# Kernel tuning notes

Measured on AMD Instinct MI355X. Metric: run time of the kernel, lower is better.

## Reference

```python
import jax, jax.numpy as jnp
import numpy as np

B, S, D = 4, 2048, 1024
H = 16
HD = D // H  # 64
MASKED_BIAS = jnp.float32(-10000.0)


def setup_inputs() -> dict:
    key = jax.random.key(0)
    ks = jax.random.split(key, 5)
    std = 0.02
    return {
        "hidden_states": jax.random.normal(ks[0], (B, S, D), jnp.float32),
        "Wq": jax.random.normal(ks[1], (D, D), jnp.float32) * std,
        "bq": jnp.zeros((D,), jnp.float32),
        "Wk": jax.random.normal(ks[2], (D, D), jnp.float32) * std,
        "bk": jnp.zeros((D,), jnp.float32),
        "Wv": jax.random.normal(ks[3], (D, D), jnp.float32) * std,
        "bv": jnp.zeros((D,), jnp.float32),
        "Wo": jax.random.normal(ks[4], (D, D), jnp.float32) * std,
        "bo": jnp.zeros((D,), jnp.float32),
    }


def _split_heads(x):
    # [B, S, D] -> [B, H, S, HD]
    return x.reshape(B, S, H, HD).transpose(0, 2, 1, 3)


def reference(hidden_states, Wq, bq, Wk, bk, Wv, bv, Wo, bo):
    q = _split_heads(hidden_states @ Wq + bq)
    k = _split_heads(hidden_states @ Wk + bk)
    v = _split_heads(hidden_states @ Wv + bv)

    # scores [B, H, S, S], scaled by sqrt(head_dim) (scale=True)
    w = jnp.einsum("bhqd,bhkd->bhqk", q, k) / jnp.sqrt(jnp.float32(HD))
    causal = jnp.tril(jnp.ones((S, S), dtype=bool))  # [S, S]
    w = jnp.where(causal[None, None], w, MASKED_BIAS)
    w = jax.nn.softmax(w, axis=-1)
    # attn_pdrop = 0.0 -> dropout is identity

    a = jnp.einsum("bhqk,bhkd->bhqd", w, v)  # [B, H, S, HD]
    a = a.transpose(0, 2, 1, 3).reshape(B, S, D)  # merge heads
    out = a @ Wo + bo
    # resid_pdrop = 0.0 -> identity
    return out
```

## Files before the change

### kernel.cpp

```cpp
#include <hip/hip_runtime.h>
#include <stdint.h>

typedef unsigned short u16;
typedef __bf16 bf16x2 __attribute__((ext_vector_type(2)));
typedef __bf16 bf16x8 __attribute__((ext_vector_type(8)));
typedef float f32x4 __attribute__((ext_vector_type(4)));
typedef float f32x16 __attribute__((ext_vector_type(16)));
typedef unsigned int u32x4 __attribute__((ext_vector_type(4)));
typedef u16 u16x8 __attribute__((ext_vector_type(8)));
typedef u16 u16x4 __attribute__((ext_vector_type(4)));

#define MFMA16(a, b, c) __builtin_amdgcn_mfma_f32_16x16x32_bf16((a), (b), (c), 0, 0, 0)
#define MFMA32(a, b, c) __builtin_amdgcn_mfma_f32_32x32x16_bf16((a), (b), (c), 0, 0, 0)

#define QSCALE 0.18033688011112042f

#if defined(__has_builtin)
#if __has_builtin(__builtin_amdgcn_exp2f)
#define EXP2(x) __builtin_amdgcn_exp2f(x)
#endif
#endif
#ifndef EXP2
#define EXP2(x) __expf((x) * 0.6931471805599453f)
#endif

__device__ __forceinline__ u16 f2bf(float f) {
  return __builtin_bit_cast(u16, (__bf16)f);
}

__device__ __forceinline__ unsigned cvtpk(float lo, float hi) {
  bf16x2 t;
  t[0] = (__bf16)lo;
  t[1] = (__bf16)hi;
  return __builtin_bit_cast(unsigned, t);
}

__device__ __forceinline__ bf16x8 load_frag(const u16* lds_base, int byteoff) {
  u32x4 v = *(const u32x4*)((const char*)lds_base + byteoff);
  return __builtin_bit_cast(bf16x8, v);
}

#define GLOAD_LDS16(gp, lp)                                                        \
  __builtin_amdgcn_global_load_lds((const __attribute__((address_space(1))) void*)(gp), \
                                   (__attribute__((address_space(3))) void*)(lp), 16, 0, 0)

template <int ROWS>
__device__ __forceinline__ void stage_tile(const u16* __restrict__ src, int ld, u16* lds,
                                           int tid) {
  constexpr int SLOTS = ROWS * 8;
#pragma unroll
  for (int it = 0; it < SLOTS / 256; ++it) {
    const int s = it * 256 + tid;
    const int row = s >> 3;
    const int seg = (s & 7) ^ (row & 7);
    const u16* g = src + row * ld + seg * 8;
    u16* l = lds + (it * 256 + (tid & ~63)) * 8;
    GLOAD_LDS16(g, l);
  }
}


__global__ __launch_bounds__(256) void cvt_x(const float* __restrict__ in,
                                             u16* __restrict__ out) {
  const int i = (int)blockIdx.x * 256 + (int)threadIdx.x;
  const float4 a = ((const float4*)in)[2 * i];
  const float4 b = ((const float4*)in)[2 * i + 1];
  u16x8 o;
  o[0] = f2bf(a.x); o[1] = f2bf(a.y); o[2] = f2bf(a.z); o[3] = f2bf(a.w);
  o[4] = f2bf(b.x); o[5] = f2bf(b.y); o[6] = f2bf(b.z); o[7] = f2bf(b.w);
  ((u16x8*)out)[i] = o;
}

__global__ __launch_bounds__(256) void cvt_w_t4(const float* __restrict__ W0,
                                                const float* __restrict__ W1,
                                                const float* __restrict__ W2,
                                                const float* __restrict__ W3,
                                                u16* __restrict__ T0, u16* __restrict__ T1,
                                                u16* __restrict__ T2, u16* __restrict__ T3) {
  const int z = (int)blockIdx.z;
  const float* W = z == 0 ? W0 : (z == 1 ? W1 : (z == 2 ? W2 : W3));
  u16* Wt = z == 0 ? T0 : (z == 1 ? T1 : (z == 2 ? T2 : T3));

  __shared__ u16 t[64][65];
  const int tid = (int)threadIdx.x;
  const int r = tid >> 2;
  const int cs = (tid & 3) * 16;
  const int tr = (int)blockIdx.y * 64;
  const int tc = (int)blockIdx.x * 64;
#pragma unroll
  for (int i = 0; i < 16; i += 4) {
    const float4 v = *(const float4*)&W[(size_t)(tr + r) * 1024 + tc + cs + i];
    t[r][cs + i + 0] = f2bf(v.x);
    t[r][cs + i + 1] = f2bf(v.y);
    t[r][cs + i + 2] = f2bf(v.z);
    t[r][cs + i + 3] = f2bf(v.w);
  }
  __syncthreads();
  u16 tmp[16];
#pragma unroll
  for (int i = 0; i < 16; ++i) tmp[i] = t[cs + i][r];
  u16x8 o0, o1;
#pragma unroll
  for (int i = 0; i < 8; ++i) { o0[i] = tmp[i]; o1[i] = tmp[8 + i]; }
  *(u16x8*)&Wt[(size_t)(tc + r) * 1024 + tr + cs] = o0;
  *(u16x8*)&Wt[(size_t)(tc + r) * 1024 + tr + cs + 8] = o1;
}


__device__ __forceinline__ size_t vfrag_addr(int row, int col) {
  const int b = row >> 11, s = row & 2047;
  const int h = col >> 6, d = col & 63;
  return ((size_t)((b * 16 + h) * 32 + (s >> 6))) * 4096 + (size_t)(d >> 5) * 2048 +
         (size_t)((s & 63) >> 4) * 512 + (size_t)((d & 31) | (((s >> 3) & 1) << 5)) * 8 +
         (s & 7);
}

__device__ __forceinline__ size_t kfrag_addr(int row, int col) {
  const int b = row >> 11, s = row & 2047;
  const int h = col >> 6, d = col & 63;
  return ((size_t)((b * 16 + h) * 64 + (s >> 5))) * 2048 + (size_t)(d >> 4) * 512 +
         (size_t)((s & 31) | (((d >> 3) & 1) << 5)) * 8 + (d & 7);
}


__device__ __forceinline__ void compute_tile(const u16* __restrict__ buf, int wm, int wn,
                                             int lr, int lg, f32x4 (&acc)[4][4]) {
#pragma unroll
  for (int ks = 0; ks < 2; ++ks) {
    bf16x8 af[4], bf[4];
#pragma unroll
    for (int i = 0; i < 4; ++i) {
      const int ar = wm * 64 + i * 16 + lr;
      af[i] = load_frag(buf, ar * 128 + ((ks * 64 + lg * 16) ^ ((ar & 7) << 4)));
      const int br = wn * 64 + i * 16 + lr;
      bf[i] = load_frag(buf + 8192, br * 128 + ((ks * 64 + lg * 16) ^ ((br & 7) << 4)));
    }
#pragma unroll
    for (int mf = 0; mf < 4; ++mf)
#pragma unroll
      for (int nf = 0; nf < 4; ++nf) acc[mf][nf] = MFMA16(af[mf], bf[nf], acc[mf][nf]);
  }
}

__device__ __forceinline__ void gemm_core(const u16* __restrict__ Abase,
                                          const u16* __restrict__ Bbase, u16* lds, int tid,
                                          int wm, int wn, int lr, int lg,
                                          f32x4 (&acc)[4][4]) {
  constexpr int K = 1024;
  stage_tile<128>(Abase, K, lds, tid);
  stage_tile<128>(Bbase, K, lds + 8192, tid);
  __syncthreads();
  int cur = 0;
#pragma unroll 1
  for (int k0 = 64; k0 < K; k0 += 64) {
    u16* nbuf = lds + (cur ^ 1) * 16384;
    stage_tile<128>(Abase + k0, K, nbuf, tid);
    stage_tile<128>(Bbase + k0, K, nbuf + 8192, tid);
    compute_tile(lds + cur * 16384, wm, wn, lr, lg, acc);
    __syncthreads();
    cur ^= 1;
  }
  compute_tile(lds + cur * 16384, wm, wn, lr, lg, acc);
}


__global__ __launch_bounds__(256) void gemm_qkv(const u16* __restrict__ A,
                                                const u16* __restrict__ Bq,
                                                const u16* __restrict__ Bk,
                                                const u16* __restrict__ Bv,
                                                const float* __restrict__ bq,
                                                const float* __restrict__ bk,
                                                const float* __restrict__ bv,
                                                u16* __restrict__ Qo, u16* __restrict__ Ko,
                                                u16* __restrict__ Vo) {
  __shared__ __align__(16) u16 lds[32768];
  const int tid = (int)threadIdx.x;
  const int w = tid >> 6, lane = tid & 63;
  const int wm = w >> 1, wn = w & 1;
  const int lr = lane & 15, lg = lane >> 4;
  const int g = (int)blockIdx.x;
  const int m_idx = g >> 3, nt = g & 7;
  const int mt = (int)blockIdx.y;

  const u16* Bt = m_idx == 0 ? Bq : (m_idx == 1 ? Bk : Bv);
  const float* bias = m_idx == 0 ? bq : (m_idx == 1 ? bk : bv);

  f32x4 acc[4][4] = {};
  gemm_core(A + (size_t)mt * 128 * 1024, Bt + (size_t)nt * 128 * 1024, lds, tid, wm, wn, lr,
            lg, acc);

#pragma unroll
  for (int mf = 0; mf < 4; ++mf) {
#pragma unroll
    for (int nf = 0; nf < 4; ++nf) {
      const int col = nt * 128 + wn * 64 + nf * 16 + lr;
      const float bv2 = bias[col];
#pragma unroll
      for (int r = 0; r < 4; ++r) {
        const int row = mt * 128 + wm * 64 + mf * 16 + lg * 4 + r;
        const float v = acc[mf][nf][r] + bv2;
        if (m_idx == 0) {
          Qo[(size_t)row * 1024 + col] = f2bf(v * QSCALE);
        } else if (m_idx == 1) {
          Ko[kfrag_addr(row, col)] = f2bf(v);
        } else {
          Vo[vfrag_addr(row, col)] = f2bf(v);
        }
      }
    }
  }
}


__global__ __launch_bounds__(256) void gemm_out(const u16* __restrict__ A,
                                                const u16* __restrict__ Bt,
                                                const float* __restrict__ bias,
                                                float* __restrict__ Cout) {
  __shared__ __align__(16) u16 lds[32768];
  const int tid = (int)threadIdx.x;
  const int w = tid >> 6, lane = tid & 63;
  const int wm = w >> 1, wn = w & 1;
  const int lr = lane & 15, lg = lane >> 4;
  const int mt = (int)blockIdx.y, nt = (int)blockIdx.x;

  f32x4 acc[4][4] = {};
  gemm_core(A + (size_t)mt * 128 * 1024, Bt + (size_t)nt * 128 * 1024, lds, tid, wm, wn, lr,
            lg, acc);

#pragma unroll
  for (int mf = 0; mf < 4; ++mf) {
#pragma unroll
    for (int nf = 0; nf < 4; ++nf) {
      const int col = nt * 128 + wn * 64 + nf * 16 + lr;
      const float bv = bias[col];
#pragma unroll
      for (int r = 0; r < 4; ++r) {
        const int row = mt * 128 + wm * 64 + mf * 16 + lg * 4 + r;
        Cout[(size_t)row * 1024 + col] = acc[mf][nf][r] + bv;
      }
    }
  }
}


__device__ __forceinline__ void loadK(bf16x8 (&kf)[2][4], const u16* __restrict__ p) {
#pragma unroll
  for (int sb = 0; sb < 2; ++sb)
#pragma unroll
    for (int dk = 0; dk < 4; ++dk)
      kf[sb][dk] = *(const bf16x8*)(p + sb * 2048 + dk * 512);
}

__device__ __forceinline__ void attn_tile(const bf16x8 (&kf)[2][4],
                                          const u16* __restrict__ vp_tile,
                                          const bf16x8 (&qf)[4], const int hi,
                                          const bool masked, const int tmask, f32x16& o0,
                                          f32x16& o1, float& m_run, float& l_run) {
  bf16x8 vf[2][4];
#pragma unroll
  for (int db = 0; db < 2; ++db)
#pragma unroll
    for (int ks = 0; ks < 4; ++ks)
      vf[db][ks] = *(const bf16x8*)(vp_tile + db * 2048 + ks * 512);

  f32x16 p0 = {}, p1 = {};
#pragma unroll
  for (int dk = 0; dk < 4; ++dk) {
    p0 = MFMA32(kf[0][dk], qf[dk], p0);
    p1 = MFMA32(kf[1][dk], qf[dk], p1);
  }

  if (masked) {
#pragma unroll
    for (int r = 0; r < 16; ++r) {
      const int kl = (r & 3) + 8 * (r >> 2) + 4 * hi;
      if (kl > tmask) p0[r] = -1.0e30f;
      if (kl + 32 > tmask) p1[r] = -1.0e30f;
    }
  }

  float mx = -3.0e38f;
#pragma unroll
  for (int r = 0; r < 16; ++r) mx = fmaxf(mx, fmaxf(p0[r], p1[r]));
  mx = fmaxf(mx, __shfl_xor(mx, 32));

  if (__any(mx > m_run + 11.5416f)) {
    const float mnew = fmaxf(m_run, mx);
    const float alpha = EXP2(m_run - mnew);
    m_run = mnew;
    l_run *= alpha;
#pragma unroll
    for (int r = 0; r < 16; ++r) { o0[r] *= alpha; o1[r] *= alpha; }
  }

  float rs = 0.0f;
#pragma unroll
  for (int r = 0; r < 16; ++r) {
    p0[r] = EXP2(p0[r] - m_run);
    p1[r] = EXP2(p1[r] - m_run);
    rs += p0[r] + p1[r];
  }
  rs += __shfl_xor(rs, 32);
  l_run += rs;

  unsigned c[16];
#pragma unroll
  for (int j = 0; j < 8; ++j) {
    c[j] = cvtpk(p0[2 * j], p0[2 * j + 1]);
    c[8 + j] = cvtpk(p1[2 * j], p1[2 * j + 1]);
  }
  bf16x8 pf[4];
#pragma unroll
  for (int ks = 0; ks < 4; ++ks) {
    const int base = (ks >> 1) * 8 + (ks & 1) * 4;
    auto s0 = __builtin_amdgcn_permlane32_swap(c[base + 0], c[base + 2], false, false);
    auto s1 = __builtin_amdgcn_permlane32_swap(c[base + 1], c[base + 3], false, false);
    u32x4 wv;
    wv[0] = s0[0];
    wv[1] = s1[0];
    wv[2] = s0[1];
    wv[3] = s1[1];
    pf[ks] = __builtin_bit_cast(bf16x8, wv);
  }

#pragma unroll
  for (int ks = 0; ks < 4; ++ks) {
    o0 = MFMA32(vf[0][ks], pf[ks], o0);
    o1 = MFMA32(vf[1][ks], pf[ks], o1);
  }
}

__global__ __launch_bounds__(64) void attn_fwd(const u16* __restrict__ Qb,
                                               const u16* __restrict__ Kf,
                                               const u16* __restrict__ Vf,
                                               u16* __restrict__ Ab) {
  const int lane = (int)threadIdx.x;
  const int ln = lane & 31, hi = lane >> 5;

  const int id = (int)blockIdx.x;
  const int xcd = id & 7;
  const int bh = (xcd << 3) | ((id >> 3) & 7);
  const int pair = id >> 6;
  const int b = bh >> 4, h = bh & 15;

  const u16* kp = Kf + (size_t)bh * 131072 + lane * 8;
  const u16* vp = Vf + (size_t)bh * 131072 + lane * 8;

#pragma unroll 1
  for (int pass = 0; pass < 2; ++pass) {
    const int qs = pass ? 63 - pair : pair;
    const int wq = qs * 32;
    const int qrow = wq + ln;

    const u16* qp = Qb + (size_t)(b * 2048 + qrow) * 1024 + h * 64 + hi * 8;
    bf16x8 qf[4];
#pragma unroll
    for (int dk = 0; dk < 4; ++dk) qf[dk] = *(const bf16x8*)(qp + dk * 16);

    f32x16 o0 = {}, o1 = {};
    float m_run = -3.0e38f, l_run = 0.0f;

    const int nt = (qs >> 1) + 1;
    bf16x8 kA[2][4], kB[2][4];
    loadK(kA, kp);
    int i = 0;
    while (i + 2 <= nt) {
      loadK(kB, kp + (size_t)(i + 1) * 4096);
      attn_tile(kA, vp + (size_t)i * 4096, qf, hi, false, 0, o0, o1, m_run, l_run);
      const int nx = (i + 2 < nt) ? i + 2 : i + 1;
      loadK(kA, kp + (size_t)nx * 4096);
      attn_tile(kB, vp + (size_t)(i + 1) * 4096, qf, hi, i + 2 == nt, qrow - (i + 1) * 64,
                o0, o1, m_run, l_run);
      i += 2;
    }
    if (i < nt)
      attn_tile(kA, vp + (size_t)i * 4096, qf, hi, true, qrow - i * 64, o0, o1, m_run,
                l_run);

    const float inv = 1.0f / l_run;
    u16* op = Ab + (size_t)(b * 2048 + qrow) * 1024 + h * 64;
#pragma unroll
    for (int rr = 0; rr < 4; ++rr) {
      u16x4 s0v, s1v;
#pragma unroll
      for (int cc = 0; cc < 4; ++cc) {
        s0v[cc] = f2bf(o0[rr * 4 + cc] * inv);
        s1v[cc] = f2bf(o1[rr * 4 + cc] * inv);
      }
      *(u16x4*)(op + rr * 8 + hi * 4) = s0v;
      *(u16x4*)(op + 32 + rr * 8 + hi * 4) = s1v;
    }
  }
}


extern "C" void kernel_launch(void* const* d_in, const int* in_sizes, int n_in, void* d_out,
                              int out_size, void* d_ws, size_t ws_size, hipStream_t stream) {
  const float* X = (const float*)d_in[0];
  const float* Wq = (const float*)d_in[1];
  const float* bq = (const float*)d_in[2];
  const float* Wk = (const float*)d_in[3];
  const float* bk = (const float*)d_in[4];
  const float* Wv = (const float*)d_in[5];
  const float* bv = (const float*)d_in[6];
  const float* Wo = (const float*)d_in[7];
  const float* bo = (const float*)d_in[8];
  float* out = (float*)d_out;

  u16* ws = (u16*)d_ws;
  u16* Xb = ws;
  u16* Wqt = Xb + 8388608;
  u16* Wkt = Wqt + 1048576;
  u16* Wvt = Wkt + 1048576;
  u16* Wot = Wvt + 1048576;
  u16* Qb = Wot + 1048576;
  u16* Kf = Qb + 8388608;
  u16* Vf = Kf + 8388608;
  u16* Ab = Vf + 8388608;

  cvt_x<<<4096, 256, 0, stream>>>(X, Xb);
  dim3 wtg(16, 16, 4);
  cvt_w_t4<<<wtg, 256, 0, stream>>>(Wq, Wk, Wv, Wo, Wqt, Wkt, Wvt, Wot);

  dim3 qkvg(24, 64);
  gemm_qkv<<<qkvg, 256, 0, stream>>>(Xb, Wqt, Wkt, Wvt, bq, bk, bv, Qb, Kf, Vf);

  attn_fwd<<<2048, 64, 0, stream>>>(Qb, Kf, Vf, Ab);

  dim3 gg(8, 64);
  gemm_out<<<gg, 256, 0, stream>>>(Ab, Wot, bo, out);
}
```

Baseline: 173.8 us.

## Group four attention waves per block and split softmax reductions into independent chains

The attention kernel now launches 1024 blocks of 256 threads, with each of the four waves handling a different 32-row query strip of the same head. The second pass moves to a neighbouring head (rr^1) instead of reusing the same head. The intent is better co-scheduling and possibly more K/V cache sharing across waves in a block. The row max and row sum reductions are split into multiple independent accumulators to shorten dependency chains. The risk is that a block's waves have unequal work and that the new head mapping changes load balance.

```diff
diff --git a/kernel.cpp b/kernel.cpp
--- a/kernel.cpp
+++ b/kernel.cpp
@@ -279,9 +279,13 @@
     }
   }
 
-  float mx = -3.0e38f;
-#pragma unroll
-  for (int r = 0; r < 16; ++r) mx = fmaxf(mx, fmaxf(p0[r], p1[r]));
+  float mx0 = -3.0e38f, mx1 = -3.0e38f;
+#pragma unroll
+  for (int r = 0; r < 16; r += 2) {
+    mx0 = fmaxf(mx0, fmaxf(p0[r], p0[r + 1]));
+    mx1 = fmaxf(mx1, fmaxf(p1[r], p1[r + 1]));
+  }
+  float mx = fmaxf(mx0, mx1);
   mx = fmaxf(mx, __shfl_xor(mx, 32));
 
   if (__any(mx > m_run + 11.5416f)) {
@@ -293,13 +297,19 @@
     for (int r = 0; r < 16; ++r) { o0[r] *= alpha; o1[r] *= alpha; }
   }
 
-  float rs = 0.0f;
-#pragma unroll
-  for (int r = 0; r < 16; ++r) {
+  float rs0 = 0.f, rs1 = 0.f, rs2 = 0.f, rs3 = 0.f;
+#pragma unroll
+  for (int r = 0; r < 16; r += 2) {
     p0[r] = EXP2(p0[r] - m_run);
+    p0[r + 1] = EXP2(p0[r + 1] - m_run);
     p1[r] = EXP2(p1[r] - m_run);
-    rs += p0[r] + p1[r];
-  }
+    p1[r + 1] = EXP2(p1[r + 1] - m_run);
+    rs0 += p0[r];
+    rs1 += p0[r + 1];
+    rs2 += p1[r];
+    rs3 += p1[r + 1];
+  }
+  float rs = (rs0 + rs1) + (rs2 + rs3);
   rs += __shfl_xor(rs, 32);
   l_run += rs;
 
@@ -330,25 +340,24 @@
   }
 }
 
-__global__ __launch_bounds__(64) void attn_fwd(const u16* __restrict__ Qb,
-                                               const u16* __restrict__ Kf,
-                                               const u16* __restrict__ Vf,
-                                               u16* __restrict__ Ab) {
-  const int lane = (int)threadIdx.x;
+__global__ __launch_bounds__(256, 4) void attn_fwd(const u16* __restrict__ Qb,
+                                                   const u16* __restrict__ Kf,
+                                                   const u16* __restrict__ Vf,
+                                                   u16* __restrict__ Ab) {
+  const int tid = (int)threadIdx.x;
+  const int w = tid >> 6, lane = tid & 63;
   const int ln = lane & 31, hi = lane >> 5;
 
   const int id = (int)blockIdx.x;
   const int xcd = id & 7;
-  const int bh = (xcd << 3) | ((id >> 3) & 7);
-  const int pair = id >> 6;
-  const int b = bh >> 4, h = bh & 15;
-
-  const u16* kp = Kf + (size_t)bh * 131072 + lane * 8;
-  const u16* vp = Vf + (size_t)bh * 131072 + lane * 8;
+  const int rr = (id >> 3) & 7;
+  const int qs0 = (id >> 6) * 4 + w;
 
 #pragma unroll 1
   for (int pass = 0; pass < 2; ++pass) {
-    const int qs = pass ? 63 - pair : pair;
+    const int bh = (xcd << 3) | (pass ? (rr ^ 1) : rr);
+    const int qs = pass ? 63 - qs0 : qs0;
+    const int b = bh >> 4, h = bh & 15;
     const int wq = qs * 32;
     const int qrow = wq + ln;
 
@@ -356,6 +365,9 @@
     bf16x8 qf[4];
 #pragma unroll
     for (int dk = 0; dk < 4; ++dk) qf[dk] = *(const bf16x8*)(qp + dk * 16);
+
+    const u16* kp = Kf + (size_t)bh * 131072 + lane * 8;
+    const u16* vp = Vf + (size_t)bh * 131072 + lane * 8;
 
     f32x16 o0 = {}, o1 = {};
     float m_run = -3.0e38f, l_run = 0.0f;
@@ -380,15 +392,15 @@
     const float inv = 1.0f / l_run;
     u16* op = Ab + (size_t)(b * 2048 + qrow) * 1024 + h * 64;
 #pragma unroll
-    for (int rr = 0; rr < 4; ++rr) {
+    for (int rr2 = 0; rr2 < 4; ++rr2) {
       u16x4 s0v, s1v;
 #pragma unroll
       for (int cc = 0; cc < 4; ++cc) {
-        s0v[cc] = f2bf(o0[rr * 4 + cc] * inv);
-        s1v[cc] = f2bf(o1[rr * 4 + cc] * inv);
+        s0v[cc] = f2bf(o0[rr2 * 4 + cc] * inv);
+        s1v[cc] = f2bf(o1[rr2 * 4 + cc] * inv);
       }
-      *(u16x4*)(op + rr * 8 + hi * 4) = s0v;
-      *(u16x4*)(op + 32 + rr * 8 + hi * 4) = s1v;
+      *(u16x4*)(op + rr2 * 8 + hi * 4) = s0v;
+      *(u16x4*)(op + 32 + rr2 * 8 + hi * 4) = s1v;
     }
   }
 }
@@ -425,7 +437,7 @@
   dim3 qkvg(24, 64);
   gemm_qkv<<<qkvg, 256, 0, stream>>>(Xb, Wqt, Wkt, Wvt, bq, bk, bv, Qb, Kf, Vf);
 
-  attn_fwd<<<2048, 64, 0, stream>>>(Qb, Kf, Vf, Ab);
+  attn_fwd<<<1024, 256, 0, stream>>>(Qb, Kf, Vf, Ab);
 
   dim3 gg(8, 64);
   gemm_out<<<gg, 256, 0, stream>>>(Ab, Wot, bo, out);
```

Result: slower. 639.0 us (+267.7%).

## Process two query stripes per wave in one pass sharing K/V tile loads

Applied to the files above, without the earlier changes.

Instead of handling the short and long query stripes in two sequential passes, each wave now keeps both stripes' Q fragments and accumulators live and walks the K/V tiles once. Each loaded K and V tile feeds both stripes, so the K/V loads for the shorter stripe's range are no longer repeated. The stripe pairing changes from (pair, 63-pair) to (m, m+32), which keeps per-block work balanced. The cost is roughly double the accumulator and Q registers, which may reduce occupancy or cause spills, and a branch inside the tile loop.

```diff
diff --git a/kernel.cpp b/kernel.cpp
--- a/kernel.cpp
+++ b/kernel.cpp
@@ -251,18 +251,12 @@
       kf[sb][dk] = *(const bf16x8*)(p + sb * 2048 + dk * 512);
 }
 
-__device__ __forceinline__ void attn_tile(const bf16x8 (&kf)[2][4],
-                                          const u16* __restrict__ vp_tile,
-                                          const bf16x8 (&qf)[4], const int hi,
-                                          const bool masked, const int tmask, f32x16& o0,
-                                          f32x16& o1, float& m_run, float& l_run) {
-  bf16x8 vf[2][4];
-#pragma unroll
-  for (int db = 0; db < 2; ++db)
-#pragma unroll
-    for (int ks = 0; ks < 4; ++ks)
-      vf[db][ks] = *(const bf16x8*)(vp_tile + db * 2048 + ks * 512);
-
+__device__ __forceinline__ void process_stripe(const bf16x8 (&kf)[2][4],
+                                               const bf16x8 (&vf)[2][4],
+                                               const bf16x8 (&qf)[4], const int hi,
+                                               const bool masked, const int tmask,
+                                               f32x16& o0, f32x16& o1, float& m_run,
+                                               float& l_run) {
   f32x16 p0 = {}, p1 = {};
 #pragma unroll
   for (int dk = 0; dk < 4; ++dk) {
@@ -330,6 +324,25 @@
   }
 }
 
+__device__ __forceinline__ void tile2(const bf16x8 (&kf)[2][4],
+                                      const u16* __restrict__ vp_tile,
+                                      const bf16x8 (&qfA)[4], const bf16x8 (&qfB)[4],
+                                      const int hi, const int i, const int ntA,
+                                      const int ntB, const int qrowA, const int qrowB,
+                                      f32x16& oA0, f32x16& oA1, float& mA, float& lA,
+                                      f32x16& oB0, f32x16& oB1, float& mB, float& lB) {
+  bf16x8 vf[2][4];
+#pragma unroll
+  for (int db = 0; db < 2; ++db)
+#pragma unroll
+    for (int ks = 0; ks < 4; ++ks)
+      vf[db][ks] = *(const bf16x8*)(vp_tile + db * 2048 + ks * 512);
+
+  process_stripe(kf, vf, qfB, hi, i == ntB - 1, qrowB - i * 64, oB0, oB1, mB, lB);
+  if (i < ntA)
+    process_stripe(kf, vf, qfA, hi, i == ntA - 1, qrowA - i * 64, oA0, oA1, mA, lA);
+}
+
 __global__ __launch_bounds__(64) void attn_fwd(const u16* __restrict__ Qb,
                                                const u16* __restrict__ Kf,
                                                const u16* __restrict__ Vf,
@@ -340,56 +353,65 @@
   const int id = (int)blockIdx.x;
   const int xcd = id & 7;
   const int bh = (xcd << 3) | ((id >> 3) & 7);
-  const int pair = id >> 6;
+  const int m = 31 - (id >> 6);
   const int b = bh >> 4, h = bh & 15;
+  const int qsA = m, qsB = m + 32;
+  const int qrowA = qsA * 32 + ln, qrowB = qsB * 32 + ln;
+
+  bf16x8 qfA[4], qfB[4];
+  {
+    const u16* qpA = Qb + (size_t)(b * 2048 + qrowA) * 1024 + h * 64 + hi * 8;
+    const u16* qpB = Qb + (size_t)(b * 2048 + qrowB) * 1024 + h * 64 + hi * 8;
+#pragma unroll
+    for (int dk = 0; dk < 4; ++dk) {
+      qfA[dk] = *(const bf16x8*)(qpA + dk * 16);
+      qfB[dk] = *(const bf16x8*)(qpB + dk * 16);
+    }
+  }
 
   const u16* kp = Kf + (size_t)bh * 131072 + lane * 8;
   const u16* vp = Vf + (size_t)bh * 131072 + lane * 8;
 
-#pragma unroll 1
-  for (int pass = 0; pass < 2; ++pass) {
-    const int qs = pass ? 63 - pair : pair;
-    const int wq = qs * 32;
-    const int qrow = wq + ln;
-
-    const u16* qp = Qb + (size_t)(b * 2048 + qrow) * 1024 + h * 64 + hi * 8;
-    bf16x8 qf[4];
-#pragma unroll
-    for (int dk = 0; dk < 4; ++dk) qf[dk] = *(const bf16x8*)(qp + dk * 16);
-
-    f32x16 o0 = {}, o1 = {};
-    float m_run = -3.0e38f, l_run = 0.0f;
-
-    const int nt = (qs >> 1) + 1;
-    bf16x8 kA[2][4], kB[2][4];
-    loadK(kA, kp);
-    int i = 0;
-    while (i + 2 <= nt) {
-      loadK(kB, kp + (size_t)(i + 1) * 4096);
-      attn_tile(kA, vp + (size_t)i * 4096, qf, hi, false, 0, o0, o1, m_run, l_run);
-      const int nx = (i + 2 < nt) ? i + 2 : i + 1;
-      loadK(kA, kp + (size_t)nx * 4096);
-      attn_tile(kB, vp + (size_t)(i + 1) * 4096, qf, hi, i + 2 == nt, qrow - (i + 1) * 64,
-                o0, o1, m_run, l_run);
-      i += 2;
-    }
-    if (i < nt)
-      attn_tile(kA, vp + (size_t)i * 4096, qf, hi, true, qrow - i * 64, o0, o1, m_run,
-                l_run);
-
-    const float inv = 1.0f / l_run;
-    u16* op = Ab + (size_t)(b * 2048 + qrow) * 1024 + h * 64;
-#pragma unroll
-    for (int rr = 0; rr < 4; ++rr) {
-      u16x4 s0v, s1v;
-#pragma unroll
-      for (int cc = 0; cc < 4; ++cc) {
-        s0v[cc] = f2bf(o0[rr * 4 + cc] * inv);
-        s1v[cc] = f2bf(o1[rr * 4 + cc] * inv);
-      }
-      *(u16x4*)(op + rr * 8 + hi * 4) = s0v;
-      *(u16x4*)(op + 32 + rr * 8 + hi * 4) = s1v;
-    }
+  f32x16 oA0 = {}, oA1 = {}, oB0 = {}, oB1 = {};
+  float mA = -3.0e38f, lA = 0.0f, mB = -3.0e38f, lB = 0.0f;
+
+  const int ntA = (qsA >> 1) + 1;
+  const int ntB = (qsB >> 1) + 1;
+
+  bf16x8 kA[2][4], kB[2][4];
+  loadK(kA, kp);
+  int i = 0;
+  while (i + 2 <= ntB) {
+    loadK(kB, kp + (size_t)(i + 1) * 4096);
+    tile2(kA, vp + (size_t)i * 4096, qfA, qfB, hi, i, ntA, ntB, qrowA, qrowB, oA0, oA1, mA,
+          lA, oB0, oB1, mB, lB);
+    const int nx = (i + 2 < ntB) ? i + 2 : i + 1;
+    loadK(kA, kp + (size_t)nx * 4096);
+    tile2(kB, vp + (size_t)(i + 1) * 4096, qfA, qfB, hi, i + 1, ntA, ntB, qrowA, qrowB, oA0,
+          oA1, mA, lA, oB0, oB1, mB, lB);
+    i += 2;
+  }
+  if (i < ntB)
+    tile2(kA, vp + (size_t)i * 4096, qfA, qfB, hi, i, ntA, ntB, qrowA, qrowB, oA0, oA1, mA,
+          lA, oB0, oB1, mB, lB);
+
+  const float invA = 1.0f / lA, invB = 1.0f / lB;
+  u16* opA = Ab + (size_t)(b * 2048 + qrowA) * 1024 + h * 64;
+  u16* opB = Ab + (size_t)(b * 2048 + qrowB) * 1024 + h * 64;
+#pragma unroll
+  for (int rr = 0; rr < 4; ++rr) {
+    u16x4 a0v, a1v, b0v, b1v;
+#pragma unroll
+    for (int cc = 0; cc < 4; ++cc) {
+      a0v[cc] = f2bf(oA0[rr * 4 + cc] * invA);
+      a1v[cc] = f2bf(oA1[rr * 4 + cc] * invA);
+      b0v[cc] = f2bf(oB0[rr * 4 + cc] * invB);
+      b1v[cc] = f2bf(oB1[rr * 4 + cc] * invB);
+    }
+    *(u16x4*)(opA + rr * 8 + hi * 4) = a0v;
+    *(u16x4*)(opA + 32 + rr * 8 + hi * 4) = a1v;
+    *(u16x4*)(opB + rr * 8 + hi * 4) = b0v;
+    *(u16x4*)(opB + 32 + rr * 8 + hi * 4) = b1v;
   }
 }
 
```

After: 177.2 us. No clear change (+2.0%).
